# Optimization experiments

Measured on AMD Instinct MI355X. Metric: run time of the kernel, lower is better.

Reference implementation:

```python
import jax, jax.numpy as jnp
import numpy as np

EPS = 1e-8


def _cdist(a, b):
    # a: [B,N,3], b: [B,M,3] -> euclidean distances [B,N,M]
    a2 = jnp.sum(a * a, axis=-1)[:, :, None]          # [B,N,1]
    b2 = jnp.sum(b * b, axis=-1)[:, None, :]          # [B,1,M]
    ab = jnp.einsum('bnd,bmd->bnm', a, b)             # [B,N,M]
    d2 = jnp.maximum(a2 + b2 - 2.0 * ab, 0.0)
    return jnp.sqrt(d2)


def setup_inputs() -> dict:
    key = jax.random.key(0)
    ks = jax.random.split(key, 8)
    B, N, M, C1, C2 = 16, 4096, 1024, 128, 256
    Cin = C1 + C2  # 384
    H1, H2 = 256, 128
    return {
        'xyz1': jax.random.normal(ks[0], (B, N, 3), dtype=jnp.float32),
        'xyz2': jax.random.normal(ks[1], (B, M, 3), dtype=jnp.float32),
        'points1': jax.random.normal(ks[2], (B, C1, N), dtype=jnp.float32),
        'points2': jax.random.normal(ks[3], (B, C2, M), dtype=jnp.float32),
        'W1': jax.random.normal(ks[4], (H1, Cin), dtype=jnp.float32) * (1.0 / np.sqrt(Cin)),
        'b1': jnp.zeros((H1,), dtype=jnp.float32),
        'W2': jax.random.normal(ks[5], (H2, H1), dtype=jnp.float32) * (1.0 / np.sqrt(H1)),
        'b2': jnp.zeros((H2,), dtype=jnp.float32),
    }


def reference(xyz1, xyz2, points1, points2, W1, b1, W2, b2):
    # inverse-distance weighted interpolation over ALL M source points
    dist = _cdist(xyz1, xyz2) + EPS                   # [B,N,M]
    inv = 1.0 / dist
    weight = inv / jnp.sum(inv, axis=-1, keepdims=True)
    # interpolated features: [B,N,M] @ [B,M,C2] -> [B,C2,N]
    interpolated = jnp.einsum('bnm,bcm->bcn', weight, points2)
    new_points = jnp.concatenate([points1, interpolated], axis=1)  # [B,C1+C2,N]
    # 1x1 Conv1d MLP with ReLU
    h = jax.nn.relu(jnp.einsum('oc,bcn->bon', W1, new_points) + b1[None, :, None])
    out = jax.nn.relu(jnp.einsum('oc,bcn->bon', W2, h) + b2[None, :, None])
    return out
```

## Files before the change

kernel.cpp:

```cpp
#include <hip/hip_runtime.h>
#include <math.h>

#define BBATCH 16
#define NPTS   4096
#define MPTS   1024
#define C1c    128
#define C2c    256
#define CINc   384
#define H1c    256
#define H2c    128
#define TN     64

typedef _Float16 f16x8 __attribute__((ext_vector_type(8)));
typedef _Float16 f16x4 __attribute__((ext_vector_type(4)));
typedef float    f32x4 __attribute__((ext_vector_type(4)));

#define LDI  40
#define LDXc 408
#define LDH  264

#define OFF_INV   0
#define OFF_RED   10240
#define OFF_RECIP 52224
#define SMEM_BYTES 52480

#define NFRAG_P2  (BBATCH * 32 * 16 * 64)
#define NFRAG_W1  (16 * 12 * 64)
#define NFRAG_W2  (8 * 8 * 64)
#define WS_P2S  0
#define WS_W1S  (NFRAG_P2 * 8)
#define WS_W2S  (WS_W1S + NFRAG_W1 * 8)
#define WS_F16_TOTAL (WS_W2S + NFRAG_W2 * 8)

__global__ __launch_bounds__(256) void cvt_swz(
    const float* __restrict__ p2, const float* __restrict__ W1,
    const float* __restrict__ W2, _Float16* __restrict__ ws)
{
    const int t = blockIdx.x * 256 + threadIdx.x;
    const float* src;
    _Float16* dst;
    if (t < NFRAG_P2) {
        const int lane = t & 63, wt = (t >> 6) & 15, s = (t >> 10) & 31, b = t >> 15;
        const int c = wt * 16 + (lane & 15);
        const int m = s * 32 + (lane >> 4) * 8;
        src = p2 + ((size_t)(b * C2c + c)) * MPTS + m;
        dst = ws + WS_P2S + (size_t)t * 8;
    } else if (t < NFRAG_P2 + NFRAG_W1) {
        const int u = t - NFRAG_P2;
        const int lane = u & 63, kc = (u >> 6) % 12, wt = (u >> 6) / 12;
        const int o = wt * 16 + (lane & 15);
        const int k = kc * 32 + (lane >> 4) * 8;
        src = W1 + (size_t)o * CINc + k;
        dst = ws + WS_W1S + (size_t)u * 8;
    } else {
        const int v = t - NFRAG_P2 - NFRAG_W1;
        const int lane = v & 63, oc = (v >> 6) & 7, wt2 = v >> 9;
        const int o = wt2 * 16 + (lane & 15);
        const int k = oc * 32 + (lane >> 4) * 8;
        src = W2 + (size_t)o * H1c + k;
        dst = ws + WS_W2S + (size_t)v * 8;
    }
    const float4 a0 = *(const float4*)(src);
    const float4 a1 = *(const float4*)(src + 4);
    f16x8 h;
    h[0] = (_Float16)a0.x; h[1] = (_Float16)a0.y; h[2] = (_Float16)a0.z; h[3] = (_Float16)a0.w;
    h[4] = (_Float16)a1.x; h[5] = (_Float16)a1.y; h[6] = (_Float16)a1.z; h[7] = (_Float16)a1.w;
    *(f16x8*)dst = h;
}

template <bool F16P>
__global__ __launch_bounds__(256, 3) void fp_mfma6(
    const float* __restrict__ xyz1, const float* __restrict__ xyz2,
    const float* __restrict__ p1,   const float* __restrict__ p2,
    const float* __restrict__ W1,   const float* __restrict__ b1v,
    const float* __restrict__ W2,   const float* __restrict__ b2v,
    const _Float16* __restrict__ p2s, const _Float16* __restrict__ W1s,
    const _Float16* __restrict__ W2s,
    float* __restrict__ out)
{
    __shared__ __align__(16) char smem[SMEM_BYTES];
    _Float16* s_inv   = (_Float16*)(smem + OFF_INV);
    float*    s_red   = (float*)(smem + OFF_RED);
    float*    s_recip = (float*)(smem + OFF_RECIP);
    _Float16* s_X     = (_Float16*)smem;
    _Float16* s_H     = (_Float16*)smem;

    const int tid  = threadIdx.x;
    const int w    = tid >> 6;
    const int L    = tid & 63;
    const int quad = L >> 4;
    const int l16  = L & 15;

    const int id = blockIdx.x;
    const int b  = (id & 7) * 2 + ((id >> 3) & 1);
    const int n0 = (id >> 4) * TN;

    const float* __restrict__ z2b = xyz2 + (size_t)b * MPTS * 3;
    const float* __restrict__ p2b = p2   + (size_t)b * C2c * MPTS;
    const _Float16* __restrict__ p2sb =
        F16P ? (p2s + (((size_t)b * 32 * 16 + (size_t)w * 4) * 64 + L) * 8) : (const _Float16*)nullptr;

    const float x1x = xyz1[((size_t)b * NPTS + n0 + L) * 3 + 0];
    const float x1y = xyz1[((size_t)b * NPTS + n0 + L) * 3 + 1];
    const float x1z = xyz1[((size_t)b * NPTS + n0 + L) * 3 + 2];

    f32x4 acc[4][4];
    #pragma unroll
    for (int ct = 0; ct < 4; ++ct)
        #pragma unroll
        for (int nt = 0; nt < 4; ++nt)
            acc[ct][nt] = (f32x4){0.f, 0.f, 0.f, 0.f};

    float ssum = 0.f;
    f16x8 Aa[2][4];

    auto loadA = [&](int s, f16x8 dst[4]) {
        if (F16P) {
            const _Float16* ap = p2sb + (size_t)s * (16 * 64 * 8);
            #pragma unroll
            for (int ct = 0; ct < 4; ++ct)
                dst[ct] = *(const f16x8*)(ap + (size_t)ct * (64 * 8));
        } else {
            const float* ap = p2b + (size_t)(w * 64 + l16) * MPTS + s * 32 + quad * 8;
            #pragma unroll
            for (int ct = 0; ct < 4; ++ct) {
                const float4 a0 = *(const float4*)(ap + (size_t)ct * (16 * MPTS));
                const float4 a1 = *(const float4*)(ap + (size_t)ct * (16 * MPTS) + 4);
                f16x8 h;
                h[0] = (_Float16)a0.x; h[1] = (_Float16)a0.y; h[2] = (_Float16)a0.z; h[3] = (_Float16)a0.w;
                h[4] = (_Float16)a1.x; h[5] = (_Float16)a1.y; h[6] = (_Float16)a1.z; h[7] = (_Float16)a1.w;
                dst[ct] = h;
            }
        }
    };

    auto gen = [&](int s) {
        const float* zp = z2b + (size_t)(s * 32 + w * 8) * 3;
        f32x4 zr[6];
        #pragma unroll
        for (int j = 0; j < 6; ++j) zr[j] = ((const f32x4*)zp)[j];
        const float* zv = (const float*)zr;
        f16x8 iv;
        #pragma unroll
        for (int i = 0; i < 8; ++i) {
            const float dx = x1x - zv[3 * i + 0];
            const float dy = x1y - zv[3 * i + 1];
            const float dz = x1z - zv[3 * i + 2];
            const float d2 = fmaf(dx, dx, fmaf(dy, dy, fmaf(dz, dz, 1e-12f)));
            const float inv = __builtin_amdgcn_rsqf(d2);
            ssum += inv;
            iv[i] = (_Float16)inv;
        }
        *(f16x8*)(s_inv + (s & 1) * (64 * LDI) + L * LDI + w * 8) = iv;
    };

    loadA(0, Aa[0]);
    gen(0);
    __syncthreads();

    #pragma unroll 2
    for (int s = 0; s < 32; ++s) {
        const int cur = s & 1;
        if (s + 1 < 32) {
            loadA(s + 1, Aa[cur ^ 1]);
            gen(s + 1);
        }
        const _Float16* bb = s_inv + cur * (64 * LDI) + l16 * LDI + quad * 8;
        #pragma unroll
        for (int nt = 0; nt < 4; ++nt) {
            const f16x8 bf = *(const f16x8*)(bb + nt * (16 * LDI));
            #pragma unroll
            for (int ct = 0; ct < 4; ++ct)
                acc[ct][nt] = __builtin_amdgcn_mfma_f32_16x16x32_f16(Aa[cur][ct], bf, acc[ct][nt], 0, 0, 0);
        }
        __syncthreads();
    }

    s_red[tid] = ssum;
    __syncthreads();
    if (tid < 64)
        s_recip[tid] = 1.0f / (s_red[tid] + s_red[tid + 64] + s_red[tid + 128] + s_red[tid + 192]);
    __syncthreads();

    {
        float rn4[4];
        #pragma unroll
        for (int nt = 0; nt < 4; ++nt) rn4[nt] = s_recip[nt * 16 + l16];
        #pragma unroll
        for (int ct = 0; ct < 4; ++ct)
            #pragma unroll
            for (int nt = 0; nt < 4; ++nt) {
                const f32x4 v = acc[ct][nt];
                const float r = rn4[nt];
                f16x4 hv;
                hv[0] = (_Float16)(v[0] * r);
                hv[1] = (_Float16)(v[1] * r);
                hv[2] = (_Float16)(v[2] * r);
                hv[3] = (_Float16)(v[3] * r);
                *(f16x4*)(&s_X[(nt * 16 + l16) * LDXc + 128 + w * 64 + ct * 16 + quad * 4]) = hv;
            }
    }
    {
        const float* p1b = p1 + (size_t)b * C1c * NPTS + n0;
        #pragma unroll
        for (int cc = 0; cc < 8; ++cc) {
            const int c = w * 32 + cc * 4;
            f16x4 v;
            v[0] = (_Float16)p1b[(size_t)(c + 0) * NPTS + L];
            v[1] = (_Float16)p1b[(size_t)(c + 1) * NPTS + L];
            v[2] = (_Float16)p1b[(size_t)(c + 2) * NPTS + L];
            v[3] = (_Float16)p1b[(size_t)(c + 3) * NPTS + L];
            *(f16x4*)(&s_X[L * LDXc + c]) = v;
        }
    }
    __syncthreads();

    f32x4 hacc[4][4];
    #pragma unroll
    for (int ct = 0; ct < 4; ++ct)
        #pragma unroll
        for (int nt = 0; nt < 4; ++nt)
            hacc[ct][nt] = (f32x4){0.f, 0.f, 0.f, 0.f};

    #pragma unroll 2
    for (int kc = 0; kc < 12; ++kc) {
        f16x8 af[4];
        if (F16P) {
            const _Float16* wp = W1s + (((size_t)(w * 4) * 12 + kc) * 64 + L) * 8;
            #pragma unroll
            for (int ct = 0; ct < 4; ++ct)
                af[ct] = *(const f16x8*)(wp + (size_t)ct * (12 * 64 * 8));
        } else {
            const float* wp = W1 + (size_t)(w * 64 + l16) * CINc + kc * 32 + quad * 8;
            #pragma unroll
            for (int ct = 0; ct < 4; ++ct) {
                const float4 a0 = *(const float4*)(wp + ct * (16 * CINc));
                const float4 a1 = *(const float4*)(wp + ct * (16 * CINc) + 4);
                f16x8 h;
                h[0] = (_Float16)a0.x; h[1] = (_Float16)a0.y; h[2] = (_Float16)a0.z; h[3] = (_Float16)a0.w;
                h[4] = (_Float16)a1.x; h[5] = (_Float16)a1.y; h[6] = (_Float16)a1.z; h[7] = (_Float16)a1.w;
                af[ct] = h;
            }
        }
        #pragma unroll
        for (int nt = 0; nt < 4; ++nt) {
            const f16x8 bf = *(const f16x8*)(&s_X[(nt * 16 + l16) * LDXc + kc * 32 + quad * 8]);
            #pragma unroll
            for (int ct = 0; ct < 4; ++ct)
                hacc[ct][nt] = __builtin_amdgcn_mfma_f32_16x16x32_f16(af[ct], bf, hacc[ct][nt], 0, 0, 0);
        }
    }

    __syncthreads();

    {
        f32x4 bb[4];
        #pragma unroll
        for (int ct = 0; ct < 4; ++ct)
            bb[ct] = *(const f32x4*)(b1v + w * 64 + ct * 16 + quad * 4);
        #pragma unroll
        for (int ct = 0; ct < 4; ++ct)
            #pragma unroll
            for (int nt = 0; nt < 4; ++nt) {
                const f32x4 v = hacc[ct][nt];
                f16x4 hv;
                hv[0] = (_Float16)fmaxf(v[0] + bb[ct][0], 0.f);
                hv[1] = (_Float16)fmaxf(v[1] + bb[ct][1], 0.f);
                hv[2] = (_Float16)fmaxf(v[2] + bb[ct][2], 0.f);
                hv[3] = (_Float16)fmaxf(v[3] + bb[ct][3], 0.f);
                *(f16x4*)(&s_H[(nt * 16 + l16) * LDH + w * 64 + ct * 16 + quad * 4]) = hv;
            }
    }
    __syncthreads();

    f32x4 oacc[2][4];
    #pragma unroll
    for (int ct = 0; ct < 2; ++ct)
        #pragma unroll
        for (int nt = 0; nt < 4; ++nt)
            oacc[ct][nt] = (f32x4){0.f, 0.f, 0.f, 0.f};

    #pragma unroll 2
    for (int oc = 0; oc < 8; ++oc) {
        f16x8 af2[2];
        if (F16P) {
            const _Float16* wp = W2s + (((size_t)(w * 2) * 8 + oc) * 64 + L) * 8;
            #pragma unroll
            for (int ct = 0; ct < 2; ++ct)
                af2[ct] = *(const f16x8*)(wp + (size_t)ct * (8 * 64 * 8));
        } else {
            const float* wp = W2 + (size_t)(w * 32 + l16) * H1c + oc * 32 + quad * 8;
            #pragma unroll
            for (int ct = 0; ct < 2; ++ct) {
                const float4 a0 = *(const float4*)(wp + ct * (16 * H1c));
                const float4 a1 = *(const float4*)(wp + ct * (16 * H1c) + 4);
                f16x8 h;
                h[0] = (_Float16)a0.x; h[1] = (_Float16)a0.y; h[2] = (_Float16)a0.z; h[3] = (_Float16)a0.w;
                h[4] = (_Float16)a1.x; h[5] = (_Float16)a1.y; h[6] = (_Float16)a1.z; h[7] = (_Float16)a1.w;
                af2[ct] = h;
            }
        }
        #pragma unroll
        for (int nt = 0; nt < 4; ++nt) {
            const f16x8 bf = *(const f16x8*)(&s_H[(nt * 16 + l16) * LDH + oc * 32 + quad * 8]);
            #pragma unroll
            for (int ct = 0; ct < 2; ++ct)
                oacc[ct][nt] = __builtin_amdgcn_mfma_f32_16x16x32_f16(af2[ct], bf, oacc[ct][nt], 0, 0, 0);
        }
    }

    {
        f32x4 bb2[2];
        #pragma unroll
        for (int ct = 0; ct < 2; ++ct)
            bb2[ct] = *(const f32x4*)(b2v + w * 32 + ct * 16 + quad * 4);
        #pragma unroll
        for (int ct = 0; ct < 2; ++ct)
            #pragma unroll
            for (int nt = 0; nt < 4; ++nt) {
                float* op = out + ((size_t)b * H2c + w * 32 + ct * 16 + quad * 4) * NPTS
                                + n0 + nt * 16 + l16;
                #pragma unroll
                for (int j = 0; j < 4; ++j)
                    op[(size_t)j * NPTS] = fmaxf(oacc[ct][nt][j] + bb2[ct][j], 0.f);
            }
    }
}

extern "C" void kernel_launch(void* const* d_in, const int* in_sizes, int n_in,
                              void* d_out, int out_size, void* d_ws, size_t ws_size,
                              hipStream_t stream) {
    (void)in_sizes; (void)n_in; (void)out_size;
    const float* xyz1 = (const float*)d_in[0];
    const float* xyz2 = (const float*)d_in[1];
    const float* p1   = (const float*)d_in[2];
    const float* p2   = (const float*)d_in[3];
    const float* W1   = (const float*)d_in[4];
    const float* b1   = (const float*)d_in[5];
    const float* W2   = (const float*)d_in[6];
    const float* b2   = (const float*)d_in[7];
    float* out = (float*)d_out;

    const bool useh = (ws_size >= (size_t)WS_F16_TOTAL * 2);
    dim3 grid(BBATCH * (NPTS / TN));
    dim3 block(256);
    if (useh) {
        _Float16* ws = (_Float16*)d_ws;
        const int nthr = NFRAG_P2 + NFRAG_W1 + NFRAG_W2;
        cvt_swz<<<dim3(nthr / 256), dim3(256), 0, stream>>>(p2, W1, W2, ws);
        fp_mfma6<true><<<grid, block, 0, stream>>>(xyz1, xyz2, p1, p2, W1, b1, W2, b2,
                                                   ws + WS_P2S, ws + WS_W1S, ws + WS_W2S, out);
    } else {
        fp_mfma6<false><<<grid, block, 0, stream>>>(xyz1, xyz2, p1, p2, W1, b1, W2, b2,
                                                    nullptr, nullptr, nullptr, out);
    }
}
```

Measured before the change: 177.8 us.

## Split fused interp+MLP kernel into separate interpolation and MLP kernels via fp16 workspace

Splits the single fused kernel into a pre-pass that converts points1 to swizzled fp16, an interpolation kernel that writes normalized interpolated features into an fp16 MFMA-fragment buffer, and an MLP kernel that reads it. Each kernel uses less shared memory and fewer registers than the fused one, which should allow higher occupancy and simpler scheduling. In exchange it adds a round trip of the full [B,384,N] fp16 activation tensor through global memory, plus extra launches. The split path runs only when the workspace is large enough, otherwise the old fused path is used.

```diff
diff --git a/kernel.cpp b/kernel.cpp
--- a/kernel.cpp
+++ b/kernel.cpp
@@ -19,18 +19,16 @@
 #define LDXc 408
 #define LDH  264
 
-#define OFF_INV   0
-#define OFF_RED   10240
-#define OFF_RECIP 52224
-#define SMEM_BYTES 52480
-
 #define NFRAG_P2  (BBATCH * 32 * 16 * 64)
 #define NFRAG_W1  (16 * 12 * 64)
 #define NFRAG_W2  (8 * 8 * 64)
+#define NFRAG_XS  (BBATCH * 64 * 4 * 12 * 64)
 #define WS_P2S  0
 #define WS_W1S  (NFRAG_P2 * 8)
 #define WS_W2S  (WS_W1S + NFRAG_W1 * 8)
-#define WS_F16_TOTAL (WS_W2S + NFRAG_W2 * 8)
+#define WS_XS   (WS_W2S + NFRAG_W2 * 8)
+#define WS_F16_FUSED  WS_XS
+#define WS_F16_SPLIT  (WS_XS + (size_t)NFRAG_XS * 8)
 
 __global__ __launch_bounds__(256) void cvt_swz(
     const float* __restrict__ p2, const float* __restrict__ W1,
@@ -68,6 +66,257 @@
     *(f16x8*)dst = h;
 }
 
+__global__ __launch_bounds__(256) void cvt_p1(
+    const float* __restrict__ p1, _Float16* __restrict__ xs)
+{
+    const int t  = blockIdx.x * 256 + threadIdx.x;
+    const int n0 = (t & 511) * 8;
+    const int k  = (t >> 9) & 127;
+    const int b  = t >> 16;
+    const float* src = p1 + ((size_t)(b * C1c + k)) * NPTS + n0;
+    const float4 a0 = *(const float4*)(src);
+    const float4 a1 = *(const float4*)(src + 4);
+    float v[8] = {a0.x, a0.y, a0.z, a0.w, a1.x, a1.y, a1.z, a1.w};
+    const int kc = k >> 5, khi = (k >> 3) & 3, j = k & 7;
+    #pragma unroll
+    for (int i = 0; i < 8; ++i) {
+        const int n = n0 + i;
+        const int ntile = n >> 6, nt = (n >> 4) & 3;
+        const int lane = (n & 15) + khi * 16;
+        xs[((((size_t)(b * 64 + ntile) * 4 + nt) * 12 + kc) * 64 + lane) * 8 + j] = (_Float16)v[i];
+    }
+}
+
+__global__ __launch_bounds__(256, 3) void interp_k(
+    const float* __restrict__ xyz1, const float* __restrict__ xyz2,
+    const _Float16* __restrict__ p2s, _Float16* __restrict__ xs)
+{
+    __shared__ __align__(16) char smem[11520];
+    _Float16* s_inv   = (_Float16*)(smem);
+    float*    s_red   = (float*)(smem + 10240);
+    float*    s_recip = (float*)(smem + 11264);
+
+    const int tid  = threadIdx.x;
+    const int w    = tid >> 6;
+    const int L    = tid & 63;
+    const int quad = L >> 4;
+    const int l16  = L & 15;
+
+    const int id    = blockIdx.x;
+    const int b     = (id & 7) * 2 + ((id >> 3) & 1);
+    const int ntile = id >> 4;
+    const int n0    = ntile * TN;
+
+    const float* __restrict__ z2b = xyz2 + (size_t)b * MPTS * 3;
+    const _Float16* __restrict__ p2sb =
+        p2s + (((size_t)b * 32 * 16 + (size_t)w * 4) * 64 + L) * 8;
+
+    const float x1x = xyz1[((size_t)b * NPTS + n0 + L) * 3 + 0];
+    const float x1y = xyz1[((size_t)b * NPTS + n0 + L) * 3 + 1];
+    const float x1z = xyz1[((size_t)b * NPTS + n0 + L) * 3 + 2];
+
+    f32x4 acc[4][4];
+    #pragma unroll
+    for (int ct = 0; ct < 4; ++ct)
+        #pragma unroll
+        for (int nt = 0; nt < 4; ++nt)
+            acc[ct][nt] = (f32x4){0.f, 0.f, 0.f, 0.f};
+
+    float ssum = 0.f;
+    f16x8 Aa[2][4];
+
+    auto loadA = [&](int s, f16x8 dst[4]) {
+        const _Float16* ap = p2sb + (size_t)s * (16 * 64 * 8);
+        #pragma unroll
+        for (int ct = 0; ct < 4; ++ct)
+            dst[ct] = *(const f16x8*)(ap + (size_t)ct * (64 * 8));
+    };
+
+    auto gen = [&](int s) {
+        const float* zp = z2b + (size_t)(s * 32 + w * 8) * 3;
+        f32x4 zr[6];
+        #pragma unroll
+        for (int j = 0; j < 6; ++j) zr[j] = ((const f32x4*)zp)[j];
+        const float* zv = (const float*)zr;
+        f16x8 iv;
+        #pragma unroll
+        for (int i = 0; i < 8; ++i) {
+            const float dx = x1x - zv[3 * i + 0];
+            const float dy = x1y - zv[3 * i + 1];
+            const float dz = x1z - zv[3 * i + 2];
+            const float d2 = fmaf(dx, dx, fmaf(dy, dy, fmaf(dz, dz, 1e-12f)));
+            const float inv = __builtin_amdgcn_rsqf(d2);
+            ssum += inv;
+            iv[i] = (_Float16)inv;
+        }
+        *(f16x8*)(s_inv + (s & 1) * (64 * LDI) + L * LDI + w * 8) = iv;
+    };
+
+    loadA(0, Aa[0]);
+    gen(0);
+    __syncthreads();
+
+    #pragma unroll 2
+    for (int s = 0; s < 32; ++s) {
+        const int cur = s & 1;
+        if (s + 1 < 32) {
+            loadA(s + 1, Aa[cur ^ 1]);
+            gen(s + 1);
+        }
+        const _Float16* bb = s_inv + cur * (64 * LDI) + l16 * LDI + quad * 8;
+        #pragma unroll
+        for (int nt = 0; nt < 4; ++nt) {
+            const f16x8 bf = *(const f16x8*)(bb + nt * (16 * LDI));
+            #pragma unroll
+            for (int ct = 0; ct < 4; ++ct)
+                acc[ct][nt] = __builtin_amdgcn_mfma_f32_16x16x32_f16(Aa[cur][ct], bf, acc[ct][nt], 0, 0, 0);
+        }
+        __syncthreads();
+    }
+
+    s_red[tid] = ssum;
+    __syncthreads();
+    if (tid < 64)
+        s_recip[tid] = 1.0f / (s_red[tid] + s_red[tid + 64] + s_red[tid + 128] + s_red[tid + 192]);
+    __syncthreads();
+
+    {
+        float rn4[4];
+        #pragma unroll
+        for (int nt = 0; nt < 4; ++nt) rn4[nt] = s_recip[nt * 16 + l16];
+        _Float16* xb = xs + ((size_t)(b * 64 + ntile) * 4) * (12 * 64 * 8);
+        #pragma unroll
+        for (int ct = 0; ct < 4; ++ct) {
+            const int k   = 128 + w * 64 + ct * 16 + quad * 4;
+            const int kc  = k >> 5;
+            const int kin = k & 31;
+            const int lw  = l16 + ((kin >> 3) & 3) * 16;
+            const int j   = kin & 7;
+            #pragma unroll
+            for (int nt = 0; nt < 4; ++nt) {
+                const f32x4 v = acc[ct][nt];
+                const float r = rn4[nt];
+                f16x4 hv;
+                hv[0] = (_Float16)(v[0] * r);
+                hv[1] = (_Float16)(v[1] * r);
+                hv[2] = (_Float16)(v[2] * r);
+                hv[3] = (_Float16)(v[3] * r);
+                *(f16x4*)(xb + (((size_t)nt * 12 + kc) * 64 + lw) * 8 + j) = hv;
+            }
+        }
+    }
+}
+
+__global__ __launch_bounds__(256, 3) void mlp_k(
+    const _Float16* __restrict__ W1s, const float* __restrict__ b1v,
+    const _Float16* __restrict__ W2s, const float* __restrict__ b2v,
+    const _Float16* __restrict__ xs,  float* __restrict__ out)
+{
+    __shared__ __align__(16) _Float16 s_H[64 * LDH];
+
+    const int tid  = threadIdx.x;
+    const int w    = tid >> 6;
+    const int L    = tid & 63;
+    const int quad = L >> 4;
+    const int l16  = L & 15;
+
+    const int id    = blockIdx.x;
+    const int b     = (id & 7) * 2 + ((id >> 3) & 1);
+    const int ntile = id >> 4;
+    const int n0    = ntile * TN;
+
+    const _Float16* __restrict__ xb = xs + ((size_t)(b * 64 + ntile) * 4) * (12 * 64 * 8);
+
+    f32x4 hacc[4][4];
+    #pragma unroll
+    for (int ct = 0; ct < 4; ++ct)
+        #pragma unroll
+        for (int nt = 0; nt < 4; ++nt)
+            hacc[ct][nt] = (f32x4){0.f, 0.f, 0.f, 0.f};
+
+    const _Float16* w1b = W1s + (((size_t)(w * 4)) * 12 * 64 + L) * 8;
+    #pragma unroll 2
+    for (int kc = 0; kc < 12; ++kc) {
+        f16x8 af[4], bf[4];
+        #pragma unroll
+        for (int ct = 0; ct < 4; ++ct)
+            af[ct] = *(const f16x8*)(w1b + ((size_t)ct * 12 + kc) * (64 * 8));
+        #pragma unroll
+        for (int nt = 0; nt < 4; ++nt)
+            bf[nt] = *(const f16x8*)(xb + (((size_t)nt * 12 + kc) * 64 + L) * 8);
+        #pragma unroll
+        for (int nt = 0; nt < 4; ++nt)
+            #pragma unroll
+            for (int ct = 0; ct < 4; ++ct)
+                hacc[ct][nt] = __builtin_amdgcn_mfma_f32_16x16x32_f16(af[ct], bf[nt], hacc[ct][nt], 0, 0, 0);
+    }
+
+    {
+        f32x4 bb[4];
+        #pragma unroll
+        for (int ct = 0; ct < 4; ++ct)
+            bb[ct] = *(const f32x4*)(b1v + w * 64 + ct * 16 + quad * 4);
+        #pragma unroll
+        for (int ct = 0; ct < 4; ++ct)
+            #pragma unroll
+            for (int nt = 0; nt < 4; ++nt) {
+                const f32x4 v = hacc[ct][nt];
+                f16x4 hv;
+                hv[0] = (_Float16)fmaxf(v[0] + bb[ct][0], 0.f);
+                hv[1] = (_Float16)fmaxf(v[1] + bb[ct][1], 0.f);
+                hv[2] = (_Float16)fmaxf(v[2] + bb[ct][2], 0.f);
+                hv[3] = (_Float16)fmaxf(v[3] + bb[ct][3], 0.f);
+                *(f16x4*)(&s_H[(nt * 16 + l16) * LDH + w * 64 + ct * 16 + quad * 4]) = hv;
+            }
+    }
+    __syncthreads();
+
+    f32x4 oacc[2][4];
+    #pragma unroll
+    for (int ct = 0; ct < 2; ++ct)
+        #pragma unroll
+        for (int nt = 0; nt < 4; ++nt)
+            oacc[ct][nt] = (f32x4){0.f, 0.f, 0.f, 0.f};
+
+    const _Float16* w2b = W2s + (((size_t)(w * 2)) * 8 * 64 + L) * 8;
+    #pragma unroll 2
+    for (int oc = 0; oc < 8; ++oc) {
+        f16x8 af2[2];
+        #pragma unroll
+        for (int ct = 0; ct < 2; ++ct)
+            af2[ct] = *(const f16x8*)(w2b + ((size_t)ct * 8 + oc) * (64 * 8));
+        #pragma unroll
+        for (int nt = 0; nt < 4; ++nt) {
+            const f16x8 bf = *(const f16x8*)(&s_H[(nt * 16 + l16) * LDH + oc * 32 + quad * 8]);
+            #pragma unroll
+            for (int ct = 0; ct < 2; ++ct)
+                oacc[ct][nt] = __builtin_amdgcn_mfma_f32_16x16x32_f16(af2[ct], bf, oacc[ct][nt], 0, 0, 0);
+        }
+    }
+
+    {
+        f32x4 bb2[2];
+        #pragma unroll
+        for (int ct = 0; ct < 2; ++ct)
+            bb2[ct] = *(const f32x4*)(b2v + w * 32 + ct * 16 + quad * 4);
+        #pragma unroll
+        for (int ct = 0; ct < 2; ++ct)
+            #pragma unroll
+            for (int nt = 0; nt < 4; ++nt) {
+                float* op = out + ((size_t)b * H2c + w * 32 + ct * 16 + quad * 4) * NPTS
+                                + n0 + nt * 16 + l16;
+                #pragma unroll
+                for (int j = 0; j < 4; ++j)
+                    op[(size_t)j * NPTS] = fmaxf(oacc[ct][nt][j] + bb2[ct][j], 0.f);
+            }
+    }
+}
+
+#define OFF_INV   0
+#define OFF_RED   10240
+#define OFF_RECIP 52224
+#define SMEM_BYTES 52480
+
 template <bool F16P>
 __global__ __launch_bounds__(256, 3) void fp_mfma6(
     const float* __restrict__ xyz1, const float* __restrict__ xyz2,
@@ -341,13 +590,19 @@
     const float* b2   = (const float*)d_in[7];
     float* out = (float*)d_out;
 
-    const bool useh = (ws_size >= (size_t)WS_F16_TOTAL * 2);
     dim3 grid(BBATCH * (NPTS / TN));
     dim3 block(256);
-    if (useh) {
-        _Float16* ws = (_Float16*)d_ws;
-        const int nthr = NFRAG_P2 + NFRAG_W1 + NFRAG_W2;
-        cvt_swz<<<dim3(nthr / 256), dim3(256), 0, stream>>>(p2, W1, W2, ws);
+    _Float16* ws = (_Float16*)d_ws;
+    const int nswz = NFRAG_P2 + NFRAG_W1 + NFRAG_W2;
+
+    if (ws_size >= WS_F16_SPLIT * 2) {
+        cvt_swz<<<dim3(nswz / 256), dim3(256), 0, stream>>>(p2, W1, W2, ws);
+        cvt_p1 <<<dim3(4096),       dim3(256), 0, stream>>>(p1, ws + WS_XS);
+        interp_k<<<grid, block, 0, stream>>>(xyz1, xyz2, ws + WS_P2S, ws + WS_XS);
+        mlp_k   <<<grid, block, 0, stream>>>(ws + WS_W1S, b1, ws + WS_W2S, b2,
+                                             ws + WS_XS, out);
+    } else if (ws_size >= (size_t)WS_F16_FUSED * 2) {
+        cvt_swz<<<dim3(nswz / 256), dim3(256), 0, stream>>>(p2, W1, W2, ws);
         fp_mfma6<true><<<grid, block, 0, stream>>>(xyz1, xyz2, p1, p2, W1, b1, W2, b2,
                                                    ws + WS_P2S, ws + WS_W1S, ws + WS_W2S, out);
     } else {
```

Measured after the change: 227.1 us. 1.28x slower.

## Stage xyz2 in LDS and generate weights in 128-point chunks

Applied to the files above, without the earlier changes.

Each block now copies the batch's whole xyz2 array (12 KB) into shared memory once, then reads source coordinates from LDS instead of global memory. The inverse-distance weights are produced in chunks of 128 source points, so there are 8 barriers instead of 32, and the fp16 A-fragment loads stay double-buffered per 32-column step. This trades more LDS for the weight buffer against fewer syncs and fewer global loads in the inner loop. Reused regions of shared memory for the later MLP stage must still fit.

```diff
diff --git a/kernel.cpp b/kernel.cpp
--- a/kernel.cpp
+++ b/kernel.cpp
@@ -15,12 +15,13 @@
 typedef _Float16 f16x4 __attribute__((ext_vector_type(4)));
 typedef float    f32x4 __attribute__((ext_vector_type(4)));
 
-#define LDI  40
+#define LDIW 136
 #define LDXc 408
 #define LDH  264
 
-#define OFF_INV   0
-#define OFF_RED   10240
+#define OFF_XYZ2  0
+#define OFF_INV   12288
+#define OFF_RED   47104
 #define OFF_RECIP 52224
 #define SMEM_BYTES 52480
 
@@ -69,7 +70,7 @@
 }
 
 template <bool F16P>
-__global__ __launch_bounds__(256, 3) void fp_mfma6(
+__global__ __launch_bounds__(256, 3) void fp_mfma7(
     const float* __restrict__ xyz1, const float* __restrict__ xyz2,
     const float* __restrict__ p1,   const float* __restrict__ p2,
     const float* __restrict__ W1,   const float* __restrict__ b1v,
@@ -79,6 +80,7 @@
     float* __restrict__ out)
 {
     __shared__ __align__(16) char smem[SMEM_BYTES];
+    float*    s_xyz2  = (float*)(smem + OFF_XYZ2);
     _Float16* s_inv   = (_Float16*)(smem + OFF_INV);
     float*    s_red   = (float*)(smem + OFF_RED);
     float*    s_recip = (float*)(smem + OFF_RECIP);
@@ -99,6 +101,9 @@
     const float* __restrict__ p2b = p2   + (size_t)b * C2c * MPTS;
     const _Float16* __restrict__ p2sb =
         F16P ? (p2s + (((size_t)b * 32 * 16 + (size_t)w * 4) * 64 + L) * 8) : (const _Float16*)nullptr;
+
+    for (int i = tid; i < MPTS * 3 / 4; i += 256)
+        ((f32x4*)s_xyz2)[i] = ((const f32x4*)z2b)[i];
 
     const float x1x = xyz1[((size_t)b * NPTS + n0 + L) * 3 + 0];
     const float x1y = xyz1[((size_t)b * NPTS + n0 + L) * 3 + 1];
@@ -134,44 +139,50 @@
         }
     };
 
-    auto gen = [&](int s) {
-        const float* zp = z2b + (size_t)(s * 32 + w * 8) * 3;
-        f32x4 zr[6];
-        #pragma unroll
-        for (int j = 0; j < 6; ++j) zr[j] = ((const f32x4*)zp)[j];
-        const float* zv = (const float*)zr;
-        f16x8 iv;
-        #pragma unroll
-        for (int i = 0; i < 8; ++i) {
-            const float dx = x1x - zv[3 * i + 0];
-            const float dy = x1y - zv[3 * i + 1];
-            const float dz = x1z - zv[3 * i + 2];
-            const float d2 = fmaf(dx, dx, fmaf(dy, dy, fmaf(dz, dz, 1e-12f)));
-            const float inv = __builtin_amdgcn_rsqf(d2);
-            ssum += inv;
-            iv[i] = (_Float16)inv;
-        }
-        *(f16x8*)(s_inv + (s & 1) * (64 * LDI) + L * LDI + w * 8) = iv;
+    auto gen = [&](int ss_) {
+        _Float16* buf = s_inv + (ss_ & 1) * (64 * LDIW);
+        #pragma unroll
+        for (int g = 0; g < 4; ++g) {
+            const float* zp = s_xyz2 + (size_t)(ss_ * 128 + w * 32 + g * 8) * 3;
+            f32x4 zr[6];
+            #pragma unroll
+            for (int j = 0; j < 6; ++j) zr[j] = ((const f32x4*)zp)[j];
+            const float* zv = (const float*)zr;
+            f16x8 iv;
+            #pragma unroll
+            for (int i = 0; i < 8; ++i) {
+                const float dx = x1x - zv[3 * i + 0];
+                const float dy = x1y - zv[3 * i + 1];
+                const float dz = x1z - zv[3 * i + 2];
+                const float d2 = fmaf(dx, dx, fmaf(dy, dy, fmaf(dz, dz, 1e-12f)));
+                const float inv = __builtin_amdgcn_rsqf(d2);
+                ssum += inv;
+                iv[i] = (_Float16)inv;
+            }
+            *(f16x8*)(buf + L * LDIW + w * 32 + g * 8) = iv;
+        }
     };
 
+    __syncthreads();
     loadA(0, Aa[0]);
     gen(0);
     __syncthreads();
 
-    #pragma unroll 2
-    for (int s = 0; s < 32; ++s) {
-        const int cur = s & 1;
-        if (s + 1 < 32) {
-            loadA(s + 1, Aa[cur ^ 1]);
-            gen(s + 1);
-        }
-        const _Float16* bb = s_inv + cur * (64 * LDI) + l16 * LDI + quad * 8;
-        #pragma unroll
-        for (int nt = 0; nt < 4; ++nt) {
-            const f16x8 bf = *(const f16x8*)(bb + nt * (16 * LDI));
-            #pragma unroll
-            for (int ct = 0; ct < 4; ++ct)
-                acc[ct][nt] = __builtin_amdgcn_mfma_f32_16x16x32_f16(Aa[cur][ct], bf, acc[ct][nt], 0, 0, 0);
+    for (int ss = 0; ss < 8; ++ss) {
+        if (ss + 1 < 8) gen(ss + 1);
+        const _Float16* buf = s_inv + (ss & 1) * (64 * LDIW);
+        #pragma unroll
+        for (int cc = 0; cc < 4; ++cc) {
+            const int s = ss * 4 + cc;
+            if (s + 1 < 32) loadA(s + 1, Aa[(cc + 1) & 1]);
+            const _Float16* bb = buf + l16 * LDIW + cc * 32 + quad * 8;
+            #pragma unroll
+            for (int nt = 0; nt < 4; ++nt) {
+                const f16x8 bf = *(const f16x8*)(bb + nt * (16 * LDIW));
+                #pragma unroll
+                for (int ct = 0; ct < 4; ++ct)
+                    acc[ct][nt] = __builtin_amdgcn_mfma_f32_16x16x32_f16(Aa[cc & 1][ct], bf, acc[ct][nt], 0, 0, 0);
+            }
         }
         __syncthreads();
     }
@@ -341,17 +352,16 @@
     const float* b2   = (const float*)d_in[7];
     float* out = (float*)d_out;
 
-    const bool useh = (ws_size >= (size_t)WS_F16_TOTAL * 2);
     dim3 grid(BBATCH * (NPTS / TN));
     dim3 block(256);
-    if (useh) {
+    if (ws_size >= (size_t)WS_F16_TOTAL * 2) {
         _Float16* ws = (_Float16*)d_ws;
-        const int nthr = NFRAG_P2 + NFRAG_W1 + NFRAG_W2;
-        cvt_swz<<<dim3(nthr / 256), dim3(256), 0, stream>>>(p2, W1, W2, ws);
-        fp_mfma6<true><<<grid, block, 0, stream>>>(xyz1, xyz2, p1, p2, W1, b1, W2, b2,
+        const int nswz = NFRAG_P2 + NFRAG_W1 + NFRAG_W2;
+        cvt_swz<<<dim3(nswz / 256), dim3(256), 0, stream>>>(p2, W1, W2, ws);
+        fp_mfma7<true><<<grid, block, 0, stream>>>(xyz1, xyz2, p1, p2, W1, b1, W2, b2,
                                                    ws + WS_P2S, ws + WS_W1S, ws + WS_W2S, out);
     } else {
-        fp_mfma6<false><<<grid, block, 0, stream>>>(xyz1, xyz2, p1, p2, W1, b1, W2, b2,
+        fp_mfma7<false><<<grid, block, 0, stream>>>(xyz1, xyz2, p1, p2, W1, b1, W2, b2,
                                                     nullptr, nullptr, nullptr, out);
     }
 }
```

Result: faster. 171.8 us (-3.4%).
